# Optimization experiments

Measured on AMD Instinct MI355X. Metric: run time of the kernel, lower is better.

## Reference

```python
import jax, jax.numpy as jnp
import numpy as np
from jax import lax

DILATIONS = [1, 2, 4, 8, 16, 32, 64, 128, 256, 512] * 2  # 20 layers
C = 128   # residual channels
K = 2     # kernel size


def _causal_dilated_conv(x, w, b, d):
    # x: [B, C, T], w: [2C, C, K], left-pad by d*(K-1) for causality
    pad = d * (K - 1)
    y = lax.conv_general_dilated(
        x, w, window_strides=(1,), padding=[(pad, 0)],
        rhs_dilation=(d,), dimension_numbers=('NCH', 'OIH', 'NCH'))
    return y + b[None, :, None]


def setup_inputs() -> dict:
    key = jax.random.key(0)
    ks = jax.random.split(key, 5)
    L = len(DILATIONS)
    x = jax.random.normal(ks[0], (4, C, 8192), jnp.float32)
    # 0.05 scale keeps activations stable through 20 residual layers
    w_conv = jax.random.normal(ks[1], (L, 2 * C, C, K), jnp.float32) * 0.05
    b_conv = jax.random.normal(ks[2], (L, 2 * C), jnp.float32) * 0.05
    w_out = jax.random.normal(ks[3], (L, C, C), jnp.float32) * 0.05
    b_out = jax.random.normal(ks[4], (L, C), jnp.float32) * 0.05
    return {"x": x, "w_conv": w_conv, "b_conv": b_conv,
            "w_out": w_out, "b_out": b_out}


def reference(x, w_conv, b_conv, w_out, b_out):
    """WaveNet convolution stack: per layer, causal dilated conv -> gated
    tanh*sigmoid -> 1x1 output conv; residual add; collect skips.
    Returns (output [B,C,T], skips [L,B,C,T])."""
    skips = []
    for i, d in enumerate(DILATIONS):
        h = x
        z = _causal_dilated_conv(x, w_conv[i], b_conv[i], d)  # [B, 2C, T]
        g = jnp.tanh(z[:, :C]) * jax.nn.sigmoid(z[:, C:])      # gated, [B, C, T]
        s = jnp.einsum('oc,bct->bot', w_out[i], g) + b_out[i][None, :, None]
        x = s + h  # residual connection
        skips.append(s)
    return x, jnp.stack(skips)
```

## Files before the change

### kernel.cpp

```cpp
#include <hip/hip_runtime.h>
#include <hip/hip_bf16.h>
#include <stdint.h>

using f32x4  = __attribute__((ext_vector_type(4))) float;
using bf16x8 = __attribute__((ext_vector_type(8))) short;
using bf16x4 = __attribute__((ext_vector_type(4))) short;

#define NB   4
#define NC   128
#define NT   8192
#define TL   64
#define NLAYER 20
#define GROWB 272
#define CONVN (NLAYER * 256 * 256)
#define WOUTN (NLAYER * 128 * 128)

__device__ __forceinline__ short f2b(float f) {
  union { float f; unsigned u; } v; v.f = f;
  unsigned r = v.u + 0x7FFFu + ((v.u >> 16) & 1u);
  return (short)(r >> 16);
}

__device__ __forceinline__ float b2f(short s) {
  union { unsigned u; float f; } v;
  v.u = ((unsigned)(unsigned short)s) << 16;
  return v.f;
}

__device__ __forceinline__ f32x4 mfma16(bf16x8 a, bf16x8 b, f32x4 c) {
  return __builtin_amdgcn_mfma_f32_16x16x32_bf16(a, b, c, 0, 0, 0);
}

__device__ __forceinline__ void gl_lds16(const void* g, void* l) {
  __builtin_amdgcn_global_load_lds(
      (const __attribute__((address_space(1))) void*)g,
      (__attribute__((address_space(3))) void*)l, 16, 0, 0);
}

__global__ void transpose_in(const float* __restrict__ x, short* __restrict__ xtb) {
  __shared__ float tile[64][65];
  const int t0 = blockIdx.x * 64;
  const int c0 = blockIdx.y * 64;
  const int b  = blockIdx.z;
  const int lane = threadIdx.x & 63;
  const int r4   = threadIdx.x >> 6;
  #pragma unroll
  for (int i = 0; i < 16; ++i) {
    const int cl = i * 4 + r4;
    tile[cl][lane] = x[((size_t)(b * NC + c0 + cl)) * NT + t0 + lane];
  }
  __syncthreads();
  #pragma unroll
  for (int it = 0; it < 2; ++it) {
    const int idx = it * 256 + threadIdx.x;
    const int r  = idx >> 3;
    const int gi = idx & 7;
    bf16x8 v;
    #pragma unroll
    for (int jj = 0; jj < 8; ++jj) v[jj] = f2b(tile[gi * 8 + jj][r]);
    const int t = t0 + r;
    const int ci = ((c0 >> 3) + gi) ^ (t & 7);
    *(bf16x8*)((char*)xtb + ((size_t)(b * NT + t)) * 256 + ci * 16) = v;
  }
}

__global__ void pack_weights(const float* __restrict__ w_conv,
                             const float* __restrict__ w_out,
                             short* __restrict__ wcb, short* __restrict__ wob) {
  const int idx = blockIdx.x * 256 + threadIdx.x;
  if (idx < CONVN) {
    const int k = idx & 255, o = (idx >> 8) & 255, lyr = idx >> 16;
    const int tap = k >> 7, c = k & 127;
    wcb[idx] = f2b(w_conv[(((size_t)lyr * 256 + o) * 128 + c) * 2 + tap]);
  } else if (idx < CONVN + WOUTN) {
    const int j = idx - CONVN;
    wob[j] = f2b(w_out[j]);
  }
}

__global__ __launch_bounds__(512, 4)
void wavenet_pair(const short* __restrict__ wcb,
                  const float* __restrict__ b_conv,
                  const short* __restrict__ wob,
                  const float* __restrict__ b_out,
                  const short* __restrict__ xbin,
                  short* __restrict__ xbout,
                  float* __restrict__ out,
                  int L, int d1, int d2)
{
  __shared__ char ldsY[80 * 256];
  __shared__ char ldsXG[88 * 256 + 80 * 256];
  char* X = ldsXG;
  char* G = ldsXG + 88 * 256;

  const int tid = threadIdx.x;
  const int w = tid >> 6, l = tid & 63, lh = l & 15, lq = l >> 4;
  const int o0 = 16 * w + lq * 4;
  const int uid = (blockIdx.x & 7) * 64 + (blockIdx.x >> 3);
  const int b   = uid >> 7;
  const int t0  = (uid & 127) * 64;
  const bool zhalo = (t0 == 0);
  const f32x4 fz = {0.f, 0.f, 0.f, 0.f};
  const size_t XOFFS = (size_t)NB * NC * NT;

  if (!zhalo) {
    const char* src = (const char*)xbin + ((size_t)(b * NT + t0 - 24)) * 256;
    #pragma unroll
    for (int k = 0; k < 3; ++k) {
      const int off = k * 8192 + tid * 16;
      if (off < 88 * 256) gl_lds16(src + off, X + off);
    }
  } else {
    if (tid * 16 < 6144) {
      bf16x8 z = {0, 0, 0, 0, 0, 0, 0, 0};
      *(bf16x8*)(X + tid * 16) = z;
    }
    const char* src = (const char*)xbin + ((size_t)(b * NT)) * 256;
    gl_lds16(src + tid * 16,        X + 6144 + tid * 16);
    gl_lds16(src + tid * 16 + 8192, X + 6144 + tid * 16 + 8192);
  }
  __syncthreads();

  f32x4 acc1[2][5];
  #pragma unroll
  for (int mi = 0; mi < 2; ++mi)
    #pragma unroll
    for (int nn = 0; nn < 5; ++nn) acc1[mi][nn] = fz;
  {
    const short* wl = wcb + (size_t)L * 65536;
    #pragma unroll
    for (int ks = 0; ks < 8; ++ks) {
      const bf16x8 a0 = *(const bf16x8*)(wl + (16 * w + lh) * 256 + ks * 32 + lq * 8);
      const bf16x8 a1 = *(const bf16x8*)(wl + (128 + 16 * w + lh) * 256 + ks * 32 + lq * 8);
      const int dd = (ks < 4) ? d1 : 0;
      #pragma unroll
      for (int nn = 0; nn < 5; ++nn) {
        const int p = 8 + nn * 16 + lh - dd;
        const int ci = ((ks & 3) * 4 + lq) ^ (p & 7);
        const bf16x8 bb = *(const bf16x8*)(X + p * 256 + ci * 16);
        acc1[0][nn] = mfma16(a0, bb, acc1[0][nn]);
        acc1[1][nn] = mfma16(a1, bb, acc1[1][nn]);
      }
    }
  }
  {
    float ba[4], bs[4];
    #pragma unroll
    for (int r = 0; r < 4; ++r) {
      ba[r] = b_conv[L * 256 + o0 + r];
      bs[r] = b_conv[L * 256 + 128 + o0 + r];
    }
    #pragma unroll
    for (int nn = 0; nn < 5; ++nn) {
      bf16x4 g4;
      #pragma unroll
      for (int r = 0; r < 4; ++r) {
        const float za = acc1[0][nn][r] + ba[r];
        const float zb = acc1[1][nn][r] + bs[r];
        const float th = 1.f - 2.f / (1.f + __expf(2.f * za));
        const float sg = 1.f / (1.f + __expf(-zb));
        g4[r] = f2b(th * sg);
      }
      const int q = nn * 16 + lh;
      const int ci = (o0 >> 3) ^ (q & 7);
      *(bf16x4*)(G + q * 256 + ci * 16 + (o0 & 7) * 2) = g4;
    }
  }
  __syncthreads();

  {
    f32x4 acc2[5];
    #pragma unroll
    for (int nn = 0; nn < 5; ++nn) acc2[nn] = fz;
    const short* wol = wob + (size_t)L * 16384;
    #pragma unroll
    for (int ks = 0; ks < 4; ++ks) {
      const bf16x8 a = *(const bf16x8*)(wol + (16 * w + lh) * 128 + ks * 32 + lq * 8);
      #pragma unroll
      for (int nn = 0; nn < 5; ++nn) {
        const int q = nn * 16 + lh;
        const int ci = (ks * 4 + lq) ^ (q & 7);
        const bf16x8 bb = *(const bf16x8*)(G + q * 256 + ci * 16);
        acc2[nn] = mfma16(a, bb, acc2[nn]);
      }
    }
    float bo[4];
    #pragma unroll
    for (int r = 0; r < 4; ++r) bo[r] = b_out[L * 128 + o0 + r];
    float* skipBase = out + XOFFS + ((size_t)((L * NB + b) * NC)) * NT + t0;
    #pragma unroll
    for (int nn = 0; nn < 5; ++nn) {
      const int q = nn * 16 + lh;
      const int p = q + 8;
      const int ci = (o0 >> 3) ^ (q & 7);
      const bf16x4 h4 = *(const bf16x4*)(X + p * 256 + ci * 16 + (o0 & 7) * 2);
      f32x4 s4, xn;
      #pragma unroll
      for (int r = 0; r < 4; ++r) {
        s4[r] = acc2[nn][r] + bo[r];
        xn[r] = s4[r] + b2f(h4[r]);
      }
      if (nn >= 1) {
        const int tt = (nn - 1) * 16 + lh;
        #pragma unroll
        for (int r = 0; r < 4; ++r)
          __builtin_nontemporal_store(s4[r], skipBase + (size_t)(o0 + r) * NT + tt);
      }
      bf16x4 x4;
      #pragma unroll
      for (int r = 0; r < 4; ++r) x4[r] = f2b(xn[r]);
      if (zhalo && nn == 0) { x4[0] = 0; x4[1] = 0; x4[2] = 0; x4[3] = 0; }
      *(bf16x4*)(ldsY + q * 256 + ci * 16 + (o0 & 7) * 2) = x4;
    }
  }
  __syncthreads();

  f32x4 acc1b[2][4];
  #pragma unroll
  for (int mi = 0; mi < 2; ++mi)
    #pragma unroll
    for (int n = 0; n < 4; ++n) acc1b[mi][n] = fz;
  {
    const short* wl2 = wcb + (size_t)(L + 1) * 65536;
    #pragma unroll
    for (int ks = 0; ks < 8; ++ks) {
      const bf16x8 a0 = *(const bf16x8*)(wl2 + (16 * w + lh) * 256 + ks * 32 + lq * 8);
      const bf16x8 a1 = *(const bf16x8*)(wl2 + (128 + 16 * w + lh) * 256 + ks * 32 + lq * 8);
      const int dd = (ks < 4) ? d2 : 0;
      #pragma unroll
      for (int n = 0; n < 4; ++n) {
        const int qy = 16 + n * 16 + lh - dd;
        const int ci = ((ks & 3) * 4 + lq) ^ (qy & 7);
        const bf16x8 bb = *(const bf16x8*)(ldsY + qy * 256 + ci * 16);
        acc1b[0][n] = mfma16(a0, bb, acc1b[0][n]);
        acc1b[1][n] = mfma16(a1, bb, acc1b[1][n]);
      }
    }
  }
  {
    float ba[4], bs[4];
    #pragma unroll
    for (int r = 0; r < 4; ++r) {
      ba[r] = b_conv[(L + 1) * 256 + o0 + r];
      bs[r] = b_conv[(L + 1) * 256 + 128 + o0 + r];
    }
    #pragma unroll
    for (int n = 0; n < 4; ++n) {
      bf16x4 g4;
      #pragma unroll
      for (int r = 0; r < 4; ++r) {
        const float za = acc1b[0][n][r] + ba[r];
        const float zb = acc1b[1][n][r] + bs[r];
        const float th = 1.f - 2.f / (1.f + __expf(2.f * za));
        const float sg = 1.f / (1.f + __expf(-zb));
        g4[r] = f2b(th * sg);
      }
      const int q2 = n * 16 + lh;
      const int ci = (o0 >> 3) ^ (q2 & 7);
      *(bf16x4*)(G + q2 * 256 + ci * 16 + (o0 & 7) * 2) = g4;
    }
  }
  __syncthreads();

  {
    f32x4 acc2[4];
    #pragma unroll
    for (int n = 0; n < 4; ++n) acc2[n] = fz;
    const short* wol2 = wob + (size_t)(L + 1) * 16384;
    #pragma unroll
    for (int ks = 0; ks < 4; ++ks) {
      const bf16x8 a = *(const bf16x8*)(wol2 + (16 * w + lh) * 128 + ks * 32 + lq * 8);
      #pragma unroll
      for (int n = 0; n < 4; ++n) {
        const int q2 = n * 16 + lh;
        const int ci = (ks * 4 + lq) ^ (q2 & 7);
        const bf16x8 bb = *(const bf16x8*)(G + q2 * 256 + ci * 16);
        acc2[n] = mfma16(a, bb, acc2[n]);
      }
    }
    float bo[4];
    #pragma unroll
    for (int r = 0; r < 4; ++r) bo[r] = b_out[(L + 1) * 128 + o0 + r];
    float* skipBase = out + XOFFS + ((size_t)(((L + 1) * NB + b) * NC)) * NT + t0;
    #pragma unroll
    for (int n = 0; n < 4; ++n) {
      const int tt = n * 16 + lh;
      const int q = 16 + tt;
      const int ci = (o0 >> 3) ^ (q & 7);
      const bf16x4 h4 = *(const bf16x4*)(ldsY + q * 256 + ci * 16 + (o0 & 7) * 2);
      f32x4 s4, xn;
      #pragma unroll
      for (int r = 0; r < 4; ++r) {
        s4[r] = acc2[n][r] + bo[r];
        xn[r] = s4[r] + b2f(h4[r]);
        __builtin_nontemporal_store(s4[r], skipBase + (size_t)(o0 + r) * NT + tt);
      }
      bf16x4 x4;
      #pragma unroll
      for (int r = 0; r < 4; ++r) x4[r] = f2b(xn[r]);
      *(bf16x4*)(ldsY + q * 256 + ci * 16 + (o0 & 7) * 2) = x4;
    }
  }
  __syncthreads();

  {
    char* dstBase = (char*)xbout + ((size_t)(b * NT + t0)) * 256;
    #pragma unroll
    for (int k = 0; k < 2; ++k) {
      const int idx = k * 512 + tid;
      const int r = idx >> 4, pcol = idx & 15;
      *(f32x4*)(dstBase + r * 256 + pcol * 16) =
          *(const f32x4*)(ldsY + (16 + r) * 256 + pcol * 16);
    }
  }
}

__global__ __launch_bounds__(512, 4)
void wavenet_pair6(const short* __restrict__ wcb,
                   const float* __restrict__ b_conv,
                   const short* __restrict__ wob,
                   const float* __restrict__ b_out,
                   const short* __restrict__ xbin,
                   short* __restrict__ xbout,
                   float* __restrict__ out,
                   int L, int d1, int d2)
{
  __shared__ char ldsY[96 * 256];
  __shared__ char ldsXG[112 * 256 + 96 * 256];
  char* X = ldsXG;
  char* G = ldsXG + 112 * 256;

  const int tid = threadIdx.x;
  const int w = tid >> 6, l = tid & 63, lh = l & 15, lq = l >> 4;
  const int o0 = 16 * w + lq * 4;
  const int uid = (blockIdx.x & 7) * 64 + (blockIdx.x >> 3);
  const int b   = uid >> 7;
  const int t0  = (uid & 127) * 64;
  const bool zhalo = (t0 == 0);
  const f32x4 fz = {0.f, 0.f, 0.f, 0.f};
  const size_t XOFFS = (size_t)NB * NC * NT;

  if (!zhalo) {
    const char* src = (const char*)xbin + ((size_t)(b * NT + t0 - 48)) * 256;
    #pragma unroll
    for (int k = 0; k < 4; ++k) {
      const int off = k * 8192 + tid * 16;
      if (off < 112 * 256) gl_lds16(src + off, X + off);
    }
  } else {
    if (tid * 16 < 12288) {
      bf16x8 z = {0, 0, 0, 0, 0, 0, 0, 0};
      *(bf16x8*)(X + tid * 16) = z;
      if (tid * 16 + 8192 < 12288) *(bf16x8*)(X + tid * 16 + 8192) = z;
    }
    const char* src = (const char*)xbin + ((size_t)(b * NT)) * 256;
    gl_lds16(src + tid * 16,        X + 12288 + tid * 16);
    gl_lds16(src + tid * 16 + 8192, X + 12288 + tid * 16 + 8192);
  }
  __syncthreads();

  f32x4 acc1[2][6];
  #pragma unroll
  for (int mi = 0; mi < 2; ++mi)
    #pragma unroll
    for (int nn = 0; nn < 6; ++nn) acc1[mi][nn] = fz;
  {
    const short* wl = wcb + (size_t)L * 65536;
    #pragma unroll
    for (int ks = 0; ks < 8; ++ks) {
      const bf16x8 a0 = *(const bf16x8*)(wl + (16 * w + lh) * 256 + ks * 32 + lq * 8);
      const bf16x8 a1 = *(const bf16x8*)(wl + (128 + 16 * w + lh) * 256 + ks * 32 + lq * 8);
      const int dd = (ks < 4) ? d1 : 0;
      #pragma unroll
      for (int nn = 0; nn < 6; ++nn) {
        const int p = 16 + nn * 16 + lh - dd;
        const int ci = ((ks & 3) * 4 + lq) ^ (p & 7);
        const bf16x8 bb = *(const bf16x8*)(X + p * 256 + ci * 16);
        acc1[0][nn] = mfma16(a0, bb, acc1[0][nn]);
        acc1[1][nn] = mfma16(a1, bb, acc1[1][nn]);
      }
    }
  }
  {
    float ba[4], bs[4];
    #pragma unroll
    for (int r = 0; r < 4; ++r) {
      ba[r] = b_conv[L * 256 + o0 + r];
      bs[r] = b_conv[L * 256 + 128 + o0 + r];
    }
    #pragma unroll
    for (int nn = 0; nn < 6; ++nn) {
      bf16x4 g4;
      #pragma unroll
      for (int r = 0; r < 4; ++r) {
        const float za = acc1[0][nn][r] + ba[r];
        const float zb = acc1[1][nn][r] + bs[r];
        const float th = 1.f - 2.f / (1.f + __expf(2.f * za));
        const float sg = 1.f / (1.f + __expf(-zb));
        g4[r] = f2b(th * sg);
      }
      const int q = nn * 16 + lh;
      const int ci = (o0 >> 3) ^ (q & 7);
      *(bf16x4*)(G + q * 256 + ci * 16 + (o0 & 7) * 2) = g4;
    }
  }
  __syncthreads();

  {
    f32x4 acc2[6];
    #pragma unroll
    for (int nn = 0; nn < 6; ++nn) acc2[nn] = fz;
    const short* wol = wob + (size_t)L * 16384;
    #pragma unroll
    for (int ks = 0; ks < 4; ++ks) {
      const bf16x8 a = *(const bf16x8*)(wol + (16 * w + lh) * 128 + ks * 32 + lq * 8);
      #pragma unroll
      for (int nn = 0; nn < 6; ++nn) {
        const int q = nn * 16 + lh;
        const int ci = (ks * 4 + lq) ^ (q & 7);
        const bf16x8 bb = *(const bf16x8*)(G + q * 256 + ci * 16);
        acc2[nn] = mfma16(a, bb, acc2[nn]);
      }
    }
    float bo[4];
    #pragma unroll
    for (int r = 0; r < 4; ++r) bo[r] = b_out[L * 128 + o0 + r];
    float* skipBase = out + XOFFS + ((size_t)((L * NB + b) * NC)) * NT + t0;
    #pragma unroll
    for (int nn = 0; nn < 6; ++nn) {
      const int q = nn * 16 + lh;
      const int p = q + 16;
      const int ci = (o0 >> 3) ^ (q & 7);
      const bf16x4 h4 = *(const bf16x4*)(X + p * 256 + ci * 16 + (o0 & 7) * 2);
      f32x4 s4, xn;
      #pragma unroll
      for (int r = 0; r < 4; ++r) {
        s4[r] = acc2[nn][r] + bo[r];
        xn[r] = s4[r] + b2f(h4[r]);
      }
      if (nn >= 2) {
        const int tt = (nn - 2) * 16 + lh;
        #pragma unroll
        for (int r = 0; r < 4; ++r)
          __builtin_nontemporal_store(s4[r], skipBase + (size_t)(o0 + r) * NT + tt);
      }
      bf16x4 x4;
      #pragma unroll
      for (int r = 0; r < 4; ++r) x4[r] = f2b(xn[r]);
      if (zhalo && nn < 2) { x4[0] = 0; x4[1] = 0; x4[2] = 0; x4[3] = 0; }
      *(bf16x4*)(ldsY + q * 256 + ci * 16 + (o0 & 7) * 2) = x4;
    }
  }
  __syncthreads();

  f32x4 acc1b[2][4];
  #pragma unroll
  for (int mi = 0; mi < 2; ++mi)
    #pragma unroll
    for (int n = 0; n < 4; ++n) acc1b[mi][n] = fz;
  {
    const short* wl2 = wcb + (size_t)(L + 1) * 65536;
    #pragma unroll
    for (int ks = 0; ks < 8; ++ks) {
      const bf16x8 a0 = *(const bf16x8*)(wl2 + (16 * w + lh) * 256 + ks * 32 + lq * 8);
      const bf16x8 a1 = *(const bf16x8*)(wl2 + (128 + 16 * w + lh) * 256 + ks * 32 + lq * 8);
      const int dd = (ks < 4) ? d2 : 0;
      #pragma unroll
      for (int n = 0; n < 4; ++n) {
        const int qy = 32 + n * 16 + lh - dd;
        const int ci = ((ks & 3) * 4 + lq) ^ (qy & 7);
        const bf16x8 bb = *(const bf16x8*)(ldsY + qy * 256 + ci * 16);
        acc1b[0][n] = mfma16(a0, bb, acc1b[0][n]);
        acc1b[1][n] = mfma16(a1, bb, acc1b[1][n]);
      }
    }
  }
  {
    float ba[4], bs[4];
    #pragma unroll
    for (int r = 0; r < 4; ++r) {
      ba[r] = b_conv[(L + 1) * 256 + o0 + r];
      bs[r] = b_conv[(L + 1) * 256 + 128 + o0 + r];
    }
    #pragma unroll
    for (int n = 0; n < 4; ++n) {
      bf16x4 g4;
      #pragma unroll
      for (int r = 0; r < 4; ++r) {
        const float za = acc1b[0][n][r] + ba[r];
        const float zb = acc1b[1][n][r] + bs[r];
        const float th = 1.f - 2.f / (1.f + __expf(2.f * za));
        const float sg = 1.f / (1.f + __expf(-zb));
        g4[r] = f2b(th * sg);
      }
      const int q2 = n * 16 + lh;
      const int ci = (o0 >> 3) ^ (q2 & 7);
      *(bf16x4*)(G + q2 * 256 + ci * 16 + (o0 & 7) * 2) = g4;
    }
  }
  __syncthreads();

  {
    f32x4 acc2[4];
    #pragma unroll
    for (int n = 0; n < 4; ++n) acc2[n] = fz;
    const short* wol2 = wob + (size_t)(L + 1) * 16384;
    #pragma unroll
    for (int ks = 0; ks < 4; ++ks) {
      const bf16x8 a = *(const bf16x8*)(wol2 + (16 * w + lh) * 128 + ks * 32 + lq * 8);
      #pragma unroll
      for (int n = 0; n < 4; ++n) {
        const int q2 = n * 16 + lh;
        const int ci = (ks * 4 + lq) ^ (q2 & 7);
        const bf16x8 bb = *(const bf16x8*)(G + q2 * 256 + ci * 16);
        acc2[n] = mfma16(a, bb, acc2[n]);
      }
    }
    float bo[4];
    #pragma unroll
    for (int r = 0; r < 4; ++r) bo[r] = b_out[(L + 1) * 128 + o0 + r];
    float* skipBase = out + XOFFS + ((size_t)(((L + 1) * NB + b) * NC)) * NT + t0;
    #pragma unroll
    for (int n = 0; n < 4; ++n) {
      const int tt = n * 16 + lh;
      const int q = 32 + tt;
      const int ci = (o0 >> 3) ^ (q & 7);
      const bf16x4 h4 = *(const bf16x4*)(ldsY + q * 256 + ci * 16 + (o0 & 7) * 2);
      f32x4 s4, xn;
      #pragma unroll
      for (int r = 0; r < 4; ++r) {
        s4[r] = acc2[n][r] + bo[r];
        xn[r] = s4[r] + b2f(h4[r]);
        __builtin_nontemporal_store(s4[r], skipBase + (size_t)(o0 + r) * NT + tt);
      }
      bf16x4 x4;
      #pragma unroll
      for (int r = 0; r < 4; ++r) x4[r] = f2b(xn[r]);
      *(bf16x4*)(ldsY + q * 256 + ci * 16 + (o0 & 7) * 2) = x4;
    }
  }
  __syncthreads();

  {
    char* dstBase = (char*)xbout + ((size_t)(b * NT + t0)) * 256;
    #pragma unroll
    for (int k = 0; k < 2; ++k) {
      const int idx = k * 512 + tid;
      const int r = idx >> 4, pcol = idx & 15;
      *(f32x4*)(dstBase + r * 256 + pcol * 16) =
          *(const f32x4*)(ldsY + (32 + r) * 256 + pcol * 16);
    }
  }
}

__global__ __launch_bounds__(512, 4)
void wavenet_layer(const short* __restrict__ wcb,
                   const float* __restrict__ b_conv,
                   const short* __restrict__ wob,
                   const float* __restrict__ b_out,
                   const short* __restrict__ xbin,
                   short* __restrict__ xbout,
                   float* __restrict__ out,
                   int layer, int dil, int last)
{
  __shared__ char ldsXC[TL * 256];
  __shared__ char ldsXP[TL * 256];
  __shared__ char ldsG[TL * GROWB];

  const int tid = threadIdx.x;
  const int w   = tid >> 6;
  const int l   = tid & 63;
  const int lh  = l & 15;
  const int lq  = l >> 4;
  const int o0  = 16 * w + lq * 4;
  const int uid = (blockIdx.x & 7) * 64 + (blockIdx.x >> 3);
  const int b   = uid >> 7;
  const int t0  = (uid & 127) * 64;

  {
    const char* xcg = (const char*)xbin + ((size_t)(b * NT + t0)) * 256;
    const int off = w * 2048 + l * 16;
    gl_lds16(xcg + off, ldsXC + off);
    gl_lds16(xcg + off + 1024, ldsXC + off + 1024);
  }
  if (t0 >= dil) {
    const char* xpg = (const char*)xbin + ((size_t)(b * NT + t0 - dil)) * 256;
    const int off = w * 2048 + l * 16;
    gl_lds16(xpg + off, ldsXP + off);
    gl_lds16(xpg + off + 1024, ldsXP + off + 1024);
  } else {
    const int row = tid >> 3, j8 = tid & 7;
    const int tp = t0 + row - dil;
    char* dst = ldsXP + row * 256;
    if (tp >= 0) {
      const char* src = (const char*)xbin + ((size_t)(b * NT + tp)) * 256;
      *(bf16x8*)(dst + j8 * 16)       = *(const bf16x8*)(src + j8 * 16);
      *(bf16x8*)(dst + j8 * 16 + 128) = *(const bf16x8*)(src + j8 * 16 + 128);
    } else {
      bf16x8 z = {0, 0, 0, 0, 0, 0, 0, 0};
      *(bf16x8*)(dst + j8 * 16)       = z;
      *(bf16x8*)(dst + j8 * 16 + 128) = z;
    }
  }
  __syncthreads();

  const f32x4 fz = {0.f, 0.f, 0.f, 0.f};
  f32x4 acc1[2][4];
  #pragma unroll
  for (int mi = 0; mi < 2; ++mi)
    #pragma unroll
    for (int n = 0; n < 4; ++n) acc1[mi][n] = fz;

  const short* wl = wcb + (size_t)layer * 65536;
  #pragma unroll
  for (int ks = 0; ks < 8; ++ks) {
    const bf16x8 a0 = *(const bf16x8*)(wl + (16 * w + lh) * 256 + ks * 32 + lq * 8);
    const bf16x8 a1 = *(const bf16x8*)(wl + (128 + 16 * w + lh) * 256 + ks * 32 + lq * 8);
    const char* base = (ks < 4) ? ldsXP : ldsXC;
    const int dd = (ks < 4) ? dil : 0;
    #pragma unroll
    for (int n = 0; n < 4; ++n) {
      const int tt = n * 16 + lh;
      const int ci = ((ks & 3) * 4 + lq) ^ ((tt - dd) & 7);
      const bf16x8 bb = *(const bf16x8*)(base + tt * 256 + ci * 16);
      acc1[0][n] = mfma16(a0, bb, acc1[0][n]);
      acc1[1][n] = mfma16(a1, bb, acc1[1][n]);
    }
  }

  {
    float ba[4], bs[4];
    #pragma unroll
    for (int r = 0; r < 4; ++r) {
      ba[r] = b_conv[layer * 256 + o0 + r];
      bs[r] = b_conv[layer * 256 + 128 + o0 + r];
    }
    #pragma unroll
    for (int n = 0; n < 4; ++n) {
      bf16x4 g4;
      #pragma unroll
      for (int r = 0; r < 4; ++r) {
        const float za = acc1[0][n][r] + ba[r];
        const float zb = acc1[1][n][r] + bs[r];
        const float th = 1.f - 2.f / (1.f + __expf(2.f * za));
        const float sg = 1.f / (1.f + __expf(-zb));
        g4[r] = f2b(th * sg);
      }
      const int tt = n * 16 + lh;
      *(bf16x4*)(ldsG + tt * GROWB + o0 * 2) = g4;
    }
  }
  __syncthreads();

  f32x4 acc2[4];
  #pragma unroll
  for (int n = 0; n < 4; ++n) acc2[n] = fz;
  const short* wol = wob + (size_t)layer * 16384;
  #pragma unroll
  for (int ks = 0; ks < 4; ++ks) {
    const bf16x8 a = *(const bf16x8*)(wol + (16 * w + lh) * 128 + ks * 32 + lq * 8);
    #pragma unroll
    for (int n = 0; n < 4; ++n) {
      const int tt = n * 16 + lh;
      const bf16x8 bb = *(const bf16x8*)(ldsG + tt * GROWB + ks * 64 + lq * 16);
      acc2[n] = mfma16(a, bb, acc2[n]);
    }
  }

  const size_t XOFFS = (size_t)NB * NC * NT;
  f32x4 xn4[4];
  {
    float bo[4];
    #pragma unroll
    for (int r = 0; r < 4; ++r) bo[r] = b_out[layer * 128 + o0 + r];
    float* skipBase = out + XOFFS + ((size_t)((layer * NB + b) * NC)) * NT + t0;
    #pragma unroll
    for (int n = 0; n < 4; ++n) {
      const int tt = n * 16 + lh;
      const int ci = (o0 >> 3) ^ (tt & 7);
      const bf16x4 h4 = *(const bf16x4*)(ldsXC + tt * 256 + ci * 16 + (o0 & 7) * 2);
      f32x4 s4, xn;
      #pragma unroll
      for (int r = 0; r < 4; ++r) {
        s4[r] = acc2[n][r] + bo[r];
        xn[r] = s4[r] + b2f(h4[r]);
        __builtin_nontemporal_store(s4[r], skipBase + (size_t)(o0 + r) * NT + tt);
      }
      if (!last) {
        bf16x4 x4;
        #pragma unroll
        for (int r = 0; r < 4; ++r) x4[r] = f2b(xn[r]);
        *(bf16x4*)(ldsXC + tt * 256 + ci * 16 + (o0 & 7) * 2) = x4;
      } else {
        xn4[n] = xn;
      }
    }
  }
  __syncthreads();

  if (!last) {
    char* dstBase = (char*)xbout + ((size_t)(b * NT + t0)) * 256;
    #pragma unroll
    for (int k = 0; k < 2; ++k) {
      const int idx = k * 512 + tid;
      const int r = idx >> 4, p = idx & 15;
      *(f32x4*)(dstBase + r * 256 + p * 16) = *(const f32x4*)(ldsXC + r * 256 + p * 16);
    }
  } else {
    #pragma unroll
    for (int n = 0; n < 4; ++n) {
      const int tt = n * 16 + lh;
      #pragma unroll
      for (int r = 0; r < 4; ++r)
        *(short*)(ldsXC + (o0 + r) * 128 + tt * 2) = f2b(xn4[n][r]);
    }
    __syncthreads();
    float* xBase = out + ((size_t)(b * NC)) * NT + t0;
    const int j16 = tid & 15;
    #pragma unroll
    for (int k = 0; k < 4; ++k) {
      const int o = k * 32 + (tid >> 4);
      const bf16x4 v = *(const bf16x4*)(ldsXC + o * 128 + j16 * 8);
      f32x4 f;
      #pragma unroll
      for (int r = 0; r < 4; ++r) f[r] = b2f(v[r]);
      __builtin_nontemporal_store(f, (f32x4*)(xBase + (size_t)o * NT + j16 * 4));
    }
  }
}

extern "C" void kernel_launch(void* const* d_in, const int* in_sizes, int n_in,
                              void* d_out, int out_size, void* d_ws, size_t ws_size,
                              hipStream_t stream) {
  const float* x      = (const float*)d_in[0];
  const float* w_conv = (const float*)d_in[1];
  const float* b_conv = (const float*)d_in[2];
  const float* w_out  = (const float*)d_in[3];
  const float* b_out  = (const float*)d_in[4];
  float* out = (float*)d_out;

  const size_t XTN = (size_t)NB * NT * NC;
  short* xb[2];
  xb[0] = (short*)d_ws;
  xb[1] = xb[0] + XTN;
  short* wcb = xb[1] + XTN;
  short* wob = wcb + CONVN;

  pack_weights<<<(CONVN + WOUTN + 255) / 256, 256, 0, stream>>>(w_conv, w_out, wcb, wob);
  transpose_in<<<dim3(NT / 64, NC / 64, NB), 256, 0, stream>>>(x, xb[0]);

  int cur = 0;
  wavenet_pair<<<dim3(512), 512, 0, stream>>>(wcb, b_conv, wob, b_out,
                                              xb[cur], xb[cur ^ 1], out, 0, 1, 2);
  cur ^= 1;
  wavenet_pair<<<dim3(512), 512, 0, stream>>>(wcb, b_conv, wob, b_out,
                                              xb[cur], xb[cur ^ 1], out, 2, 4, 8);
  cur ^= 1;
  wavenet_pair6<<<dim3(512), 512, 0, stream>>>(wcb, b_conv, wob, b_out,
                                               xb[cur], xb[cur ^ 1], out, 4, 16, 32);
  cur ^= 1;
  for (int i = 6; i <= 9; ++i) {
    wavenet_layer<<<dim3(512), 512, 0, stream>>>(
        wcb, b_conv, wob, b_out, xb[cur], xb[cur ^ 1], out, i, 1 << i, 0);
    cur ^= 1;
  }
  wavenet_pair<<<dim3(512), 512, 0, stream>>>(wcb, b_conv, wob, b_out,
                                              xb[cur], xb[cur ^ 1], out, 10, 1, 2);
  cur ^= 1;
  wavenet_pair<<<dim3(512), 512, 0, stream>>>(wcb, b_conv, wob, b_out,
                                              xb[cur], xb[cur ^ 1], out, 12, 4, 8);
  cur ^= 1;
  wavenet_pair6<<<dim3(512), 512, 0, stream>>>(wcb, b_conv, wob, b_out,
                                               xb[cur], xb[cur ^ 1], out, 14, 16, 32);
  cur ^= 1;
  for (int i = 16; i <= 19; ++i) {
    wavenet_layer<<<dim3(512), 512, 0, stream>>>(
        wcb, b_conv, wob, b_out, xb[cur], xb[cur ^ 1], out, i, 1 << (i - 10),
        (i == 19) ? 1 : 0);
    cur ^= 1;
  }
}
```

Before: 348.8 us.

## Fuse four early layers per kernel, merge prep kernels, coalesce skip stores via LDS

Replaces the two pair kernels covering dilations 1-8 with one quad kernel that runs four layers in LDS using a 32-row halo, rotating through three LDS buffers. This cuts kernel launches and global round-trips of the residual activation. The weight pack and input transpose are merged into one prep launch. Skip outputs in the pair6 and single-layer kernels are now staged through swizzled LDS and written as coalesced 16-byte rows instead of strided scalar stores. The cost is extra halo recompute and extra barriers.

Measured after the change: 332.2 us. 1.05x faster.

```diff
diff --git a/kernel.cpp b/kernel.cpp
--- a/kernel.cpp
+++ b/kernel.cpp
@@ -14,6 +14,8 @@
 #define GROWB 272
 #define CONVN (NLAYER * 256 * 256)
 #define WOUTN (NLAYER * 128 * 128)
+#define PACKB ((CONVN + WOUTN + 255) / 256)
+#define TRANB ((NT / 64) * (NC / 64) * NB)
 
 __device__ __forceinline__ short f2b(float f) {
   union { float f; unsigned u; } v; v.f = f;
@@ -37,11 +39,28 @@
       (__attribute__((address_space(3))) void*)l, 16, 0, 0);
 }
 
-__global__ void transpose_in(const float* __restrict__ x, short* __restrict__ xtb) {
+__global__ void prep(const float* __restrict__ x,
+                     const float* __restrict__ w_conv,
+                     const float* __restrict__ w_out,
+                     short* __restrict__ xtb,
+                     short* __restrict__ wcb, short* __restrict__ wob) {
   __shared__ float tile[64][65];
-  const int t0 = blockIdx.x * 64;
-  const int c0 = blockIdx.y * 64;
-  const int b  = blockIdx.z;
+  if (blockIdx.x < PACKB) {
+    const int idx = blockIdx.x * 256 + threadIdx.x;
+    if (idx < CONVN) {
+      const int k = idx & 255, o = (idx >> 8) & 255, lyr = idx >> 16;
+      const int tap = k >> 7, c = k & 127;
+      wcb[idx] = f2b(w_conv[(((size_t)lyr * 256 + o) * 128 + c) * 2 + tap]);
+    } else if (idx < CONVN + WOUTN) {
+      const int j = idx - CONVN;
+      wob[j] = f2b(w_out[j]);
+    }
+    return;
+  }
+  const int bid2 = blockIdx.x - PACKB;
+  const int t0 = (bid2 & 127) * 64;
+  const int c0 = ((bid2 >> 7) & 1) * 64;
+  const int b  = bid2 >> 8;
   const int lane = threadIdx.x & 63;
   const int r4   = threadIdx.x >> 6;
   #pragma unroll
@@ -64,34 +83,19 @@
   }
 }
 
-__global__ void pack_weights(const float* __restrict__ w_conv,
-                             const float* __restrict__ w_out,
-                             short* __restrict__ wcb, short* __restrict__ wob) {
-  const int idx = blockIdx.x * 256 + threadIdx.x;
-  if (idx < CONVN) {
-    const int k = idx & 255, o = (idx >> 8) & 255, lyr = idx >> 16;
-    const int tap = k >> 7, c = k & 127;
-    wcb[idx] = f2b(w_conv[(((size_t)lyr * 256 + o) * 128 + c) * 2 + tap]);
-  } else if (idx < CONVN + WOUTN) {
-    const int j = idx - CONVN;
-    wob[j] = f2b(w_out[j]);
-  }
-}
-
 __global__ __launch_bounds__(512, 4)
-void wavenet_pair(const short* __restrict__ wcb,
+void wavenet_quad(const short* __restrict__ wcb,
                   const float* __restrict__ b_conv,
                   const short* __restrict__ wob,
                   const float* __restrict__ b_out,
                   const short* __restrict__ xbin,
                   short* __restrict__ xbout,
                   float* __restrict__ out,
-                  int L, int d1, int d2)
+                  int L0)
 {
-  __shared__ char ldsY[80 * 256];
-  __shared__ char ldsXG[88 * 256 + 80 * 256];
-  char* X = ldsXG;
-  char* G = ldsXG + 88 * 256;
+  __shared__ char ldsX [96 * 256];
+  __shared__ char ldsYp[80 * 256];
+  __shared__ char ldsYq[80 * 256];
 
   const int tid = threadIdx.x;
   const int w = tid >> 6, l = tid & 63, lh = l & 15, lq = l >> 4;
@@ -104,204 +108,126 @@
   const size_t XOFFS = (size_t)NB * NC * NT;
 
   if (!zhalo) {
-    const char* src = (const char*)xbin + ((size_t)(b * NT + t0 - 24)) * 256;
-    #pragma unroll
-    for (int k = 0; k < 3; ++k) {
-      const int off = k * 8192 + tid * 16;
-      if (off < 88 * 256) gl_lds16(src + off, X + off);
-    }
+    const char* src = (const char*)xbin + ((size_t)(b * NT + t0 - 32)) * 256;
+    #pragma unroll
+    for (int k = 0; k < 3; ++k)
+      gl_lds16(src + k * 8192 + tid * 16, ldsX + k * 8192 + tid * 16);
   } else {
-    if (tid * 16 < 6144) {
-      bf16x8 z = {0, 0, 0, 0, 0, 0, 0, 0};
-      *(bf16x8*)(X + tid * 16) = z;
-    }
+    bf16x8 z = {0, 0, 0, 0, 0, 0, 0, 0};
+    *(bf16x8*)(ldsX + tid * 16) = z;
     const char* src = (const char*)xbin + ((size_t)(b * NT)) * 256;
-    gl_lds16(src + tid * 16,        X + 6144 + tid * 16);
-    gl_lds16(src + tid * 16 + 8192, X + 6144 + tid * 16 + 8192);
-  }
-  __syncthreads();
-
-  f32x4 acc1[2][5];
-  #pragma unroll
-  for (int mi = 0; mi < 2; ++mi)
-    #pragma unroll
-    for (int nn = 0; nn < 5; ++nn) acc1[mi][nn] = fz;
-  {
-    const short* wl = wcb + (size_t)L * 65536;
-    #pragma unroll
-    for (int ks = 0; ks < 8; ++ks) {
-      const bf16x8 a0 = *(const bf16x8*)(wl + (16 * w + lh) * 256 + ks * 32 + lq * 8);
-      const bf16x8 a1 = *(const bf16x8*)(wl + (128 + 16 * w + lh) * 256 + ks * 32 + lq * 8);
-      const int dd = (ks < 4) ? d1 : 0;
-      #pragma unroll
-      for (int nn = 0; nn < 5; ++nn) {
-        const int p = 8 + nn * 16 + lh - dd;
-        const int ci = ((ks & 3) * 4 + lq) ^ (p & 7);
-        const bf16x8 bb = *(const bf16x8*)(X + p * 256 + ci * 16);
-        acc1[0][nn] = mfma16(a0, bb, acc1[0][nn]);
-        acc1[1][nn] = mfma16(a1, bb, acc1[1][nn]);
-      }
-    }
-  }
-  {
-    float ba[4], bs[4];
-    #pragma unroll
-    for (int r = 0; r < 4; ++r) {
-      ba[r] = b_conv[L * 256 + o0 + r];
-      bs[r] = b_conv[L * 256 + 128 + o0 + r];
-    }
-    #pragma unroll
-    for (int nn = 0; nn < 5; ++nn) {
-      bf16x4 g4;
+    gl_lds16(src + tid * 16,        ldsX + 8192 + tid * 16);
+    gl_lds16(src + tid * 16 + 8192, ldsX + 8192 + tid * 16 + 8192);
+  }
+  __syncthreads();
+
+  #pragma unroll
+  for (int j = 0; j < 4; ++j) {
+    const int Lj = L0 + j;
+    const int d  = 1 << j;
+    const char* SRC = (j == 0) ? ldsX : ((j == 2) ? ldsYq : ldsYp);
+    char*       DST = (j == 1 || j == 3) ? ldsYq : ldsYp;
+    char*       G   = (j == 0) ? ldsYq : ldsX;
+    const int roff  = (j == 0) ? 16 : 0;
+    const int qb    = (j == 3) ? 16 : 0;
+    const int ntl   = (j == 3) ? 4  : 5;
+
+    f32x4 acc1[2][5];
+    #pragma unroll
+    for (int mi = 0; mi < 2; ++mi)
+      #pragma unroll
+      for (int nn = 0; nn < 5; ++nn) acc1[mi][nn] = fz;
+    {
+      const short* wl = wcb + (size_t)Lj * 65536;
+      #pragma unroll
+      for (int ks = 0; ks < 8; ++ks) {
+        const bf16x8 a0 = *(const bf16x8*)(wl + (16 * w + lh) * 256 + ks * 32 + lq * 8);
+        const bf16x8 a1 = *(const bf16x8*)(wl + (128 + 16 * w + lh) * 256 + ks * 32 + lq * 8);
+        const int dd = (ks < 4) ? d : 0;
+        #pragma unroll
+        for (int nn = 0; nn < 5; ++nn) if (nn < ntl) {
+          int sr = qb + nn * 16 + lh + roff - dd;
+          if (sr < 0) sr += 80;
+          const int ci = ((ks & 3) * 4 + lq) ^ (sr & 7);
+          const bf16x8 bb = *(const bf16x8*)(SRC + sr * 256 + ci * 16);
+          acc1[0][nn] = mfma16(a0, bb, acc1[0][nn]);
+          acc1[1][nn] = mfma16(a1, bb, acc1[1][nn]);
+        }
+      }
+    }
+    {
+      float ba[4], bs[4];
       #pragma unroll
       for (int r = 0; r < 4; ++r) {
-        const float za = acc1[0][nn][r] + ba[r];
-        const float zb = acc1[1][nn][r] + bs[r];
-        const float th = 1.f - 2.f / (1.f + __expf(2.f * za));
-        const float sg = 1.f / (1.f + __expf(-zb));
-        g4[r] = f2b(th * sg);
-      }
-      const int q = nn * 16 + lh;
-      const int ci = (o0 >> 3) ^ (q & 7);
-      *(bf16x4*)(G + q * 256 + ci * 16 + (o0 & 7) * 2) = g4;
-    }
-  }
-  __syncthreads();
-
-  {
-    f32x4 acc2[5];
-    #pragma unroll
-    for (int nn = 0; nn < 5; ++nn) acc2[nn] = fz;
-    const short* wol = wob + (size_t)L * 16384;
-    #pragma unroll
-    for (int ks = 0; ks < 4; ++ks) {
-      const bf16x8 a = *(const bf16x8*)(wol + (16 * w + lh) * 128 + ks * 32 + lq * 8);
-      #pragma unroll
-      for (int nn = 0; nn < 5; ++nn) {
-        const int q = nn * 16 + lh;
-        const int ci = (ks * 4 + lq) ^ (q & 7);
-        const bf16x8 bb = *(const bf16x8*)(G + q * 256 + ci * 16);
-        acc2[nn] = mfma16(a, bb, acc2[nn]);
-      }
-    }
-    float bo[4];
-    #pragma unroll
-    for (int r = 0; r < 4; ++r) bo[r] = b_out[L * 128 + o0 + r];
-    float* skipBase = out + XOFFS + ((size_t)((L * NB + b) * NC)) * NT + t0;
-    #pragma unroll
-    for (int nn = 0; nn < 5; ++nn) {
-      const int q = nn * 16 + lh;
-      const int p = q + 8;
-      const int ci = (o0 >> 3) ^ (q & 7);
-      const bf16x4 h4 = *(const bf16x4*)(X + p * 256 + ci * 16 + (o0 & 7) * 2);
-      f32x4 s4, xn;
-      #pragma unroll
-      for (int r = 0; r < 4; ++r) {
-        s4[r] = acc2[nn][r] + bo[r];
-        xn[r] = s4[r] + b2f(h4[r]);
-      }
-      if (nn >= 1) {
-        const int tt = (nn - 1) * 16 + lh;
+        ba[r] = b_conv[Lj * 256 + o0 + r];
+        bs[r] = b_conv[Lj * 256 + 128 + o0 + r];
+      }
+      #pragma unroll
+      for (int nn = 0; nn < 5; ++nn) if (nn < ntl) {
+        bf16x4 g4;
         #pragma unroll
-        for (int r = 0; r < 4; ++r)
-          __builtin_nontemporal_store(s4[r], skipBase + (size_t)(o0 + r) * NT + tt);
-      }
-      bf16x4 x4;
-      #pragma unroll
-      for (int r = 0; r < 4; ++r) x4[r] = f2b(xn[r]);
-      if (zhalo && nn == 0) { x4[0] = 0; x4[1] = 0; x4[2] = 0; x4[3] = 0; }
-      *(bf16x4*)(ldsY + q * 256 + ci * 16 + (o0 & 7) * 2) = x4;
-    }
-  }
-  __syncthreads();
-
-  f32x4 acc1b[2][4];
-  #pragma unroll
-  for (int mi = 0; mi < 2; ++mi)
-    #pragma unroll
-    for (int n = 0; n < 4; ++n) acc1b[mi][n] = fz;
-  {
-    const short* wl2 = wcb + (size_t)(L + 1) * 65536;
-    #pragma unroll
-    for (int ks = 0; ks < 8; ++ks) {
-      const bf16x8 a0 = *(const bf16x8*)(wl2 + (16 * w + lh) * 256 + ks * 32 + lq * 8);
-      const bf16x8 a1 = *(const bf16x8*)(wl2 + (128 + 16 * w + lh) * 256 + ks * 32 + lq * 8);
-      const int dd = (ks < 4) ? d2 : 0;
-      #pragma unroll
-      for (int n = 0; n < 4; ++n) {
-        const int qy = 16 + n * 16 + lh - dd;
-        const int ci = ((ks & 3) * 4 + lq) ^ (qy & 7);
-        const bf16x8 bb = *(const bf16x8*)(ldsY + qy * 256 + ci * 16);
-        acc1b[0][n] = mfma16(a0, bb, acc1b[0][n]);
-        acc1b[1][n] = mfma16(a1, bb, acc1b[1][n]);
-      }
-    }
-  }
-  {
-    float ba[4], bs[4];
-    #pragma unroll
-    for (int r = 0; r < 4; ++r) {
-      ba[r] = b_conv[(L + 1) * 256 + o0 + r];
-      bs[r] = b_conv[(L + 1) * 256 + 128 + o0 + r];
-    }
-    #pragma unroll
-    for (int n = 0; n < 4; ++n) {
-      bf16x4 g4;
-      #pragma unroll
-      for (int r = 0; r < 4; ++r) {
-        const float za = acc1b[0][n][r] + ba[r];
-        const float zb = acc1b[1][n][r] + bs[r];
-        const float th = 1.f - 2.f / (1.f + __expf(2.f * za));
-        const float sg = 1.f / (1.f + __expf(-zb));
-        g4[r] = f2b(th * sg);
-      }
-      const int q2 = n * 16 + lh;
-      const int ci = (o0 >> 3) ^ (q2 & 7);
-      *(bf16x4*)(G + q2 * 256 + ci * 16 + (o0 & 7) * 2) = g4;
-    }
-  }
-  __syncthreads();
-
-  {
-    f32x4 acc2[4];
-    #pragma unroll
-    for (int n = 0; n < 4; ++n) acc2[n] = fz;
-    const short* wol2 = wob + (size_t)(L + 1) * 16384;
-    #pragma unroll
-    for (int ks = 0; ks < 4; ++ks) {
-      const bf16x8 a = *(const bf16x8*)(wol2 + (16 * w + lh) * 128 + ks * 32 + lq * 8);
-      #pragma unroll
-      for (int n = 0; n < 4; ++n) {
-        const int q2 = n * 16 + lh;
-        const int ci = (ks * 4 + lq) ^ (q2 & 7);
-        const bf16x8 bb = *(const bf16x8*)(G + q2 * 256 + ci * 16);
-        acc2[n] = mfma16(a, bb, acc2[n]);
-      }
-    }
-    float bo[4];
-    #pragma unroll
-    for (int r = 0; r < 4; ++r) bo[r] = b_out[(L + 1) * 128 + o0 + r];
-    float* skipBase = out + XOFFS + ((size_t)(((L + 1) * NB + b) * NC)) * NT + t0;
-    #pragma unroll
-    for (int n = 0; n < 4; ++n) {
-      const int tt = n * 16 + lh;
-      const int q = 16 + tt;
-      const int ci = (o0 >> 3) ^ (q & 7);
-      const bf16x4 h4 = *(const bf16x4*)(ldsY + q * 256 + ci * 16 + (o0 & 7) * 2);
-      f32x4 s4, xn;
-      #pragma unroll
-      for (int r = 0; r < 4; ++r) {
-        s4[r] = acc2[n][r] + bo[r];
-        xn[r] = s4[r] + b2f(h4[r]);
-        __builtin_nontemporal_store(s4[r], skipBase + (size_t)(o0 + r) * NT + tt);
-      }
-      bf16x4 x4;
-      #pragma unroll
-      for (int r = 0; r < 4; ++r) x4[r] = f2b(xn[r]);
-      *(bf16x4*)(ldsY + q * 256 + ci * 16 + (o0 & 7) * 2) = x4;
-    }
-  }
-  __syncthreads();
+        for (int r = 0; r < 4; ++r) {
+          const float za = acc1[0][nn][r] + ba[r];
+          const float zb = acc1[1][nn][r] + bs[r];
+          const float th = 1.f - 2.f / (1.f + __expf(2.f * za));
+          const float sg = 1.f / (1.f + __expf(-zb));
+          g4[r] = f2b(th * sg);
+        }
+        const int q = qb + nn * 16 + lh;
+        const int ci = (o0 >> 3) ^ (q & 7);
+        *(bf16x4*)(G + q * 256 + ci * 16 + (o0 & 7) * 2) = g4;
+      }
+    }
+    __syncthreads();
+
+    {
+      f32x4 acc2[5];
+      #pragma unroll
+      for (int nn = 0; nn < 5; ++nn) acc2[nn] = fz;
+      const short* wol = wob + (size_t)Lj * 16384;
+      #pragma unroll
+      for (int ks = 0; ks < 4; ++ks) {
+        const bf16x8 a = *(const bf16x8*)(wol + (16 * w + lh) * 128 + ks * 32 + lq * 8);
+        #pragma unroll
+        for (int nn = 0; nn < 5; ++nn) if (nn < ntl) {
+          const int q = qb + nn * 16 + lh;
+          const int ci = (ks * 4 + lq) ^ (q & 7);
+          const bf16x8 bb = *(const bf16x8*)(G + q * 256 + ci * 16);
+          acc2[nn] = mfma16(a, bb, acc2[nn]);
+        }
+      }
+      float bo[4];
+      #pragma unroll
+      for (int r = 0; r < 4; ++r) bo[r] = b_out[Lj * 128 + o0 + r];
+      float* skipBase = out + XOFFS + ((size_t)((Lj * NB + b) * NC)) * NT + t0;
+      #pragma unroll
+      for (int nn = 0; nn < 5; ++nn) if (nn < ntl) {
+        const int q  = qb + nn * 16 + lh;
+        const int hr = q + roff;
+        const int cih = (o0 >> 3) ^ (hr & 7);
+        const bf16x4 h4 = *(const bf16x4*)(SRC + hr * 256 + cih * 16 + (o0 & 7) * 2);
+        f32x4 s4, xn;
+        #pragma unroll
+        for (int r = 0; r < 4; ++r) {
+          s4[r] = acc2[nn][r] + bo[r];
+          xn[r] = s4[r] + b2f(h4[r]);
+        }
+        if (q >= 16) {
+          const int tt = q - 16;
+          #pragma unroll
+          for (int r = 0; r < 4; ++r)
+            __builtin_nontemporal_store(s4[r], skipBase + (size_t)(o0 + r) * NT + tt);
+        }
+        bf16x4 x4;
+        #pragma unroll
+        for (int r = 0; r < 4; ++r) x4[r] = f2b(xn[r]);
+        if (zhalo && q < 16) { x4[0] = 0; x4[1] = 0; x4[2] = 0; x4[3] = 0; }
+        const int ciq = (o0 >> 3) ^ (q & 7);
+        *(bf16x4*)(DST + q * 256 + ciq * 16 + (o0 & 7) * 2) = x4;
+      }
+    }
+    __syncthreads();
+  }
 
   {
     char* dstBase = (char*)xbout + ((size_t)(b * NT + t0)) * 256;
@@ -310,7 +236,7 @@
       const int idx = k * 512 + tid;
       const int r = idx >> 4, pcol = idx & 15;
       *(f32x4*)(dstBase + r * 256 + pcol * 16) =
-          *(const f32x4*)(ldsY + (16 + r) * 256 + pcol * 16);
+          *(const f32x4*)(ldsYq + (16 + r) * 256 + pcol * 16);
     }
   }
 }
@@ -329,6 +255,7 @@
   __shared__ char ldsXG[112 * 256 + 96 * 256];
   char* X = ldsXG;
   char* G = ldsXG + 112 * 256;
+  char* S = ldsXG;
 
   const int tid = threadIdx.x;
   const int w = tid >> 6, l = tid & 63, lh = l & 15, lq = l >> 4;
@@ -406,6 +333,7 @@
   }
   __syncthreads();
 
+  f32x4 s4vL[4];
   {
     f32x4 acc2[6];
     #pragma unroll
@@ -425,7 +353,6 @@
     float bo[4];
     #pragma unroll
     for (int r = 0; r < 4; ++r) bo[r] = b_out[L * 128 + o0 + r];
-    float* skipBase = out + XOFFS + ((size_t)((L * NB + b) * NC)) * NT + t0;
     #pragma unroll
     for (int nn = 0; nn < 6; ++nn) {
       const int q = nn * 16 + lh;
@@ -438,12 +365,7 @@
         s4[r] = acc2[nn][r] + bo[r];
         xn[r] = s4[r] + b2f(h4[r]);
       }
-      if (nn >= 2) {
-        const int tt = (nn - 2) * 16 + lh;
-        #pragma unroll
-        for (int r = 0; r < 4; ++r)
-          __builtin_nontemporal_store(s4[r], skipBase + (size_t)(o0 + r) * NT + tt);
-      }
+      if (nn >= 2) s4vL[nn - 2] = s4;
       bf16x4 x4;
       #pragma unroll
       for (int r = 0; r < 4; ++r) x4[r] = f2b(xn[r]);
@@ -453,12 +375,37 @@
   }
   __syncthreads();
 
+  #pragma unroll
+  for (int nn = 0; nn < 4; ++nn) {
+    const int tt = nn * 16 + lh;
+    #pragma unroll
+    for (int r = 0; r < 4; ++r) {
+      const int o  = o0 + r;
+      const int lg = tt >> 2;
+      const int pg = (lg & 8) | ((lg ^ (o & 7)) & 7);
+      *(float*)(S + o * 256 + pg * 16 + (tt & 3) * 4) = s4vL[nn][r];
+    }
+  }
+  __syncthreads();
+
   f32x4 acc1b[2][4];
   #pragma unroll
   for (int mi = 0; mi < 2; ++mi)
     #pragma unroll
     for (int n = 0; n < 4; ++n) acc1b[mi][n] = fz;
   {
+    float* skipBase = out + XOFFS + ((size_t)((L * NB + b) * NC)) * NT + t0;
+    const int j8 = tid & 7;
+    #pragma unroll
+    for (int half = 0; half < 2; ++half) {
+      const int o = half * 64 + (tid >> 3);
+      #pragma unroll
+      for (int k = 0; k < 2; ++k) {
+        const int pg = (k * 8) | ((j8 ^ (o & 7)) & 7);
+        const f32x4 v = *(const f32x4*)(S + o * 256 + pg * 16);
+        __builtin_nontemporal_store(v, (f32x4*)(skipBase + (size_t)o * NT + j8 * 4 + k * 32));
+      }
+    }
     const short* wl2 = wcb + (size_t)(L + 1) * 65536;
     #pragma unroll
     for (int ks = 0; ks < 8; ++ks) {
@@ -475,6 +422,8 @@
       }
     }
   }
+  __syncthreads();
+
   {
     float ba[4], bs[4];
     #pragma unroll
@@ -500,6 +449,7 @@
   }
   __syncthreads();
 
+  f32x4 s4vP[4];
   {
     f32x4 acc2[4];
     #pragma unroll
@@ -519,11 +469,9 @@
     float bo[4];
     #pragma unroll
     for (int r = 0; r < 4; ++r) bo[r] = b_out[(L + 1) * 128 + o0 + r];
-    float* skipBase = out + XOFFS + ((size_t)(((L + 1) * NB + b) * NC)) * NT + t0;
     #pragma unroll
     for (int n = 0; n < 4; ++n) {
-      const int tt = n * 16 + lh;
-      const int q = 32 + tt;
+      const int q = 32 + n * 16 + lh;
       const int ci = (o0 >> 3) ^ (q & 7);
       const bf16x4 h4 = *(const bf16x4*)(ldsY + q * 256 + ci * 16 + (o0 & 7) * 2);
       f32x4 s4, xn;
@@ -531,8 +479,8 @@
       for (int r = 0; r < 4; ++r) {
         s4[r] = acc2[n][r] + bo[r];
         xn[r] = s4[r] + b2f(h4[r]);
-        __builtin_nontemporal_store(s4[r], skipBase + (size_t)(o0 + r) * NT + tt);
-      }
+      }
+      s4vP[n] = s4;
       bf16x4 x4;
       #pragma unroll
       for (int r = 0; r < 4; ++r) x4[r] = f2b(xn[r]);
@@ -541,7 +489,32 @@
   }
   __syncthreads();
 
-  {
+  #pragma unroll
+  for (int n = 0; n < 4; ++n) {
+    const int tt = n * 16 + lh;
+    #pragma unroll
+    for (int r = 0; r < 4; ++r) {
+      const int o  = o0 + r;
+      const int lg = tt >> 2;
+      const int pg = (lg & 8) | ((lg ^ (o & 7)) & 7);
+      *(float*)(S + o * 256 + pg * 16 + (tt & 3) * 4) = s4vP[n][r];
+    }
+  }
+  __syncthreads();
+
+  {
+    float* skipBase = out + XOFFS + ((size_t)(((L + 1) * NB + b) * NC)) * NT + t0;
+    const int j8 = tid & 7;
+    #pragma unroll
+    for (int half = 0; half < 2; ++half) {
+      const int o = half * 64 + (tid >> 3);
+      #pragma unroll
+      for (int k = 0; k < 2; ++k) {
+        const int pg = (k * 8) | ((j8 ^ (o & 7)) & 7);
+        const f32x4 v = *(const f32x4*)(S + o * 256 + pg * 16);
+        __builtin_nontemporal_store(v, (f32x4*)(skipBase + (size_t)o * NT + j8 * 4 + k * 32));
+      }
+    }
     char* dstBase = (char*)xbout + ((size_t)(b * NT + t0)) * 256;
     #pragma unroll
     for (int k = 0; k < 2; ++k) {
@@ -564,8 +537,10 @@
                    int layer, int dil, int last)
 {
   __shared__ char ldsXC[TL * 256];
-  __shared__ char ldsXP[TL * 256];
-  __shared__ char ldsG[TL * GROWB];
+  __shared__ char ldsSP[TL * 256 + TL * GROWB];
+  char* ldsXP = ldsSP;
+  char* ldsG  = ldsSP + TL * 256;
+  char* ldsS  = ldsSP;
 
   const int tid = threadIdx.x;
   const int w   = tid >> 6;
@@ -666,14 +641,13 @@
       acc2[n] = mfma16(a, bb, acc2[n]);
     }
   }
-
-  const size_t XOFFS = (size_t)NB * NC * NT;
+  __syncthreads();
+
   f32x4 xn4[4];
   {
     float bo[4];
     #pragma unroll
     for (int r = 0; r < 4; ++r) bo[r] = b_out[layer * 128 + o0 + r];
-    float* skipBase = out + XOFFS + ((size_t)((layer * NB + b) * NC)) * NT + t0;
     #pragma unroll
     for (int n = 0; n < 4; ++n) {
       const int tt = n * 16 + lh;
@@ -684,7 +658,13 @@
       for (int r = 0; r < 4; ++r) {
         s4[r] = acc2[n][r] + bo[r];
         xn[r] = s4[r] + b2f(h4[r]);
-        __builtin_nontemporal_store(s4[r], skipBase + (size_t)(o0 + r) * NT + tt);
+      }
+      #pragma unroll
+      for (int r = 0; r < 4; ++r) {
+        const int o  = o0 + r;
+        const int lg = tt >> 2;
+        const int pg = (lg & 8) | ((lg ^ (o & 7)) & 7);
+        *(float*)(ldsS + o * 256 + pg * 16 + (tt & 3) * 4) = s4[r];
       }
       if (!last) {
         bf16x4 x4;
@@ -698,6 +678,21 @@
   }
   __syncthreads();
 
+  const size_t XOFFS = (size_t)NB * NC * NT;
+  {
+    float* skipBase = out + XOFFS + ((size_t)((layer * NB + b) * NC)) * NT + t0;
+    const int j8 = tid & 7;
+    #pragma unroll
+    for (int half = 0; half < 2; ++half) {
+      const int o = half * 64 + (tid >> 3);
+      #pragma unroll
+      for (int k = 0; k < 2; ++k) {
+        const int pg = (k * 8) | ((j8 ^ (o & 7)) & 7);
+        const f32x4 v = *(const f32x4*)(ldsS + o * 256 + pg * 16);
+        __builtin_nontemporal_store(v, (f32x4*)(skipBase + (size_t)o * NT + j8 * 4 + k * 32));
+      }
+    }
+  }
   if (!last) {
     char* dstBase = (char*)xbout + ((size_t)(b * NT + t0)) * 256;
     #pragma unroll
@@ -707,12 +702,14 @@
       *(f32x4*)(dstBase + r * 256 + p * 16) = *(const f32x4*)(ldsXC + r * 256 + p * 16);
     }
   } else {
-    #pragma unroll
-    for (int n = 0; n < 4; ++n) {
-      const int tt = n * 16 + lh;
-      #pragma unroll
-      for (int r = 0; r < 4; ++r)
-        *(short*)(ldsXC + (o0 + r) * 128 + tt * 2) = f2b(xn4[n][r]);
+    {
+      #pragma unroll
+      for (int n = 0; n < 4; ++n) {
+        const int tt = n * 16 + lh;
+        #pragma unroll
+        for (int r = 0; r < 4; ++r)
+          *(short*)(ldsXC + (o0 + r) * 128 + tt * 2) = f2b(xn4[n][r]);
+      }
     }
     __syncthreads();
     float* xBase = out + ((size_t)(b * NC)) * NT + t0;
@@ -746,15 +743,11 @@
   short* wcb = xb[1] + XTN;
   short* wob = wcb + CONVN;
 
-  pack_weights<<<(CONVN + WOUTN + 255) / 256, 256, 0, stream>>>(w_conv, w_out, wcb, wob);
-  transpose_in<<<dim3(NT / 64, NC / 64, NB), 256, 0, stream>>>(x, xb[0]);
+  prep<<<dim3(PACKB + TRANB), 256, 0, stream>>>(x, w_conv, w_out, xb[0], wcb, wob);
 
   int cur = 0;
-  wavenet_pair<<<dim3(512), 512, 0, stream>>>(wcb, b_conv, wob, b_out,
-                                              xb[cur], xb[cur ^ 1], out, 0, 1, 2);
-  cur ^= 1;
-  wavenet_pair<<<dim3(512), 512, 0, stream>>>(wcb, b_conv, wob, b_out,
-                                              xb[cur], xb[cur ^ 1], out, 2, 4, 8);
+  wavenet_quad<<<dim3(512), 512, 0, stream>>>(wcb, b_conv, wob, b_out,
+                                              xb[cur], xb[cur ^ 1], out, 0);
   cur ^= 1;
   wavenet_pair6<<<dim3(512), 512, 0, stream>>>(wcb, b_conv, wob, b_out,
                                                xb[cur], xb[cur ^ 1], out, 4, 16, 32);
@@ -764,11 +757,8 @@
         wcb, b_conv, wob, b_out, xb[cur], xb[cur ^ 1], out, i, 1 << i, 0);
     cur ^= 1;
   }
-  wavenet_pair<<<dim3(512), 512, 0, stream>>>(wcb, b_conv, wob, b_out,
-                                              xb[cur], xb[cur ^ 1], out, 10, 1, 2);
-  cur ^= 1;
-  wavenet_pair<<<dim3(512), 512, 0, stream>>>(wcb, b_conv, wob, b_out,
-                                              xb[cur], xb[cur ^ 1], out, 12, 4, 8);
+  wavenet_quad<<<dim3(512), 512, 0, stream>>>(wcb, b_conv, wob, b_out,
+                                              xb[cur], xb[cur ^ 1], out, 10);
   cur ^= 1;
   wavenet_pair6<<<dim3(512), 512, 0, stream>>>(wcb, b_conv, wob, b_out,
                                                xb[cur], xb[cur ^ 1], out, 14, 16, 32);
```
